# Kernel tuning notes

Measured on AMD Instinct MI355X. Metric: run time of the kernel, lower is better.

Reference implementation:

```python
import jax, jax.numpy as jnp
from jax import lax
import numpy as np

N = 65536
D = 512
NUM_STEPS = 10
TIME_INTERVAL = 1.0


def setup_inputs() -> dict:
    key = jax.random.key(0)
    ks = jax.random.split(key, 8)
    s1 = 1.0 / np.sqrt(D + 1)
    s2 = 1.0 / np.sqrt(D)
    sg = 1.0 / np.sqrt(2 * D)
    return {
        "current_node_features": jax.random.normal(ks[0], (N, D), jnp.float32),
        "previous_hidden_state": jax.random.normal(ks[1], (N, D), jnp.float32),
        # torch nn.Linear layout: weight [out, in], bias [out]
        "W1": jax.random.uniform(ks[2], (D, D + 1), jnp.float32, -s1, s1),
        "b1": jax.random.uniform(ks[3], (D,), jnp.float32, -s1, s1),
        "W2": jax.random.uniform(ks[4], (D, D), jnp.float32, -s2, s2),
        "b2": jax.random.uniform(ks[5], (D,), jnp.float32, -s2, s2),
        "Wg": jax.random.uniform(ks[6], (D, 2 * D), jnp.float32, -sg, sg),
        "bg": jax.random.uniform(ks[7], (D,), jnp.float32, -sg, sg),
    }


def reference(current_node_features, previous_hidden_state, W1, b1, W2, b2, Wg, bg):
    x = current_node_features
    dt = jnp.asarray(TIME_INTERVAL / NUM_STEPS, x.dtype)
    n = x.shape[0]

    def euler_step(h, t):
        # concat time feature: [N, D+1]
        time_col = jnp.full((n, 1), t, h.dtype)
        z = jnp.concatenate([h, time_col], axis=-1)
        deriv = jnp.tanh(jnp.tanh(z @ W1.T + b1) @ W2.T + b2)
        return h + dt * deriv, None

    ts = jnp.arange(NUM_STEPS, dtype=x.dtype) * dt  # t_i = start + i*dt
    evolved, _ = lax.scan(euler_step, previous_hidden_state, ts)

    combined = jnp.concatenate([x, evolved], axis=-1)  # [N, 2D]
    gate = jax.nn.sigmoid(combined @ Wg.T + bg)
    updated = gate * evolved + (1.0 - gate) * x
    return updated, updated
```

## Files before the change

kernel.cpp:

```cpp
#include <hip/hip_runtime.h>

#define N_ROWS 65536
#define DIM    512
#define NSTEP  10

typedef float  f32x16 __attribute__((ext_vector_type(16)));
typedef float  f32x4  __attribute__((ext_vector_type(4)));
typedef short  s16x8  __attribute__((ext_vector_type(8)));
typedef __bf16 bf16x8 __attribute__((ext_vector_type(8)));
typedef unsigned int u32x2 __attribute__((ext_vector_type(2)));
typedef unsigned int u32x4 __attribute__((ext_vector_type(4)));

__device__ __forceinline__ unsigned f2bf(float f) {
  unsigned u = __float_as_uint(f);
  return (u + 0x7fffu + ((u >> 16) & 1u)) >> 16;
}
__device__ __forceinline__ unsigned pack2bf_rn(float a, float b) {
  unsigned ua = __float_as_uint(a) + 0x8000u;
  unsigned ub = __float_as_uint(b) + 0x8000u;
  return __builtin_amdgcn_perm(ub, ua, 0x07060302u);
}
#define LOG2E_X2 2.885390081777927f
#define LOG2E    1.442695040888963f
__device__ __forceinline__ float ftanh(float x) {
  float t = __builtin_amdgcn_exp2f(x * LOG2E_X2);
  float r = __builtin_amdgcn_rcpf(1.0f + t);
  return __builtin_fmaf(-2.0f, r, 1.0f);
}
__device__ __forceinline__ float fsigm(float x) {
  float t = __builtin_amdgcn_exp2f(-x * LOG2E);
  return __builtin_amdgcn_rcpf(1.0f + t);
}
__device__ __forceinline__ void mfma(f32x16& c, s16x8 a, s16x8 b) {
  c = __builtin_amdgcn_mfma_f32_32x32x16_bf16(
        __builtin_bit_cast(bf16x8, a), __builtin_bit_cast(bf16x8, b), c, 0, 0, 0);
}

__global__ void pack_frags_kernel(const float* __restrict__ src, int row_stride,
                                  int col_off, unsigned short* __restrict__ dst) {
  const int idx = blockIdx.x * 256 + threadIdx.x;
  const int l    = idx & 63;
  const int frag = idx >> 6;
  const int otg  = frag >> 5;
  const int ks   = frag & 31;
  const int o = otg * 32 + (l & 31);
  const int k = ks * 16 + (l >> 5) * 8;
  const float* p = src + (size_t)o * row_stride + col_off + k;
  s16x8 v;
#pragma unroll
  for (int i = 0; i < 8; ++i) v[i] = (short)f2bf(p[i]);
  *reinterpret_cast<s16x8*>(dst + (size_t)idx * 8) = v;
}

__global__ void c1_kernel(const float* __restrict__ W1, const float* __restrict__ b1,
                          float* __restrict__ c1) {
  const int o = threadIdx.x;
  const float wt = W1[(size_t)o * 513 + 512];
  const float bb = b1[o];
  for (int s = 0; s < NSTEP; ++s)
    c1[s * DIM + o] = bb + ((float)s * 0.1f) * wt;
}

__global__ __launch_bounds__(512, 2)
void ode_fused(const float* __restrict__ x, const float* __restrict__ h0,
               const float* __restrict__ b2, const float* __restrict__ bg,
               const s16x8* __restrict__ w1f, const s16x8* __restrict__ w2f,
               const s16x8* __restrict__ wgaf, const s16x8* __restrict__ wgbf,
               const float* __restrict__ c1, float* __restrict__ out)
{
  __shared__ char ldsT[64 * 1024];

  const int tid = threadIdx.x;
  const int w   = tid >> 6;
  const int l   = tid & 63;
  const int lm  = l & 31;
  const int h5  = l >> 5;
  const int m0  = blockIdx.x << 6;
  const int ow  = w << 6;
  const unsigned lbyte = (unsigned)l << 4;

  {
#pragma unroll
    for (int q = 0; q < 8; ++q) {
      const int f  = (w << 3) | q;
      const int ks = f >> 1;
      const int mt = f & 1;
      const float* src = h0 + (size_t)(m0 + (mt << 5) + lm) * DIM + (ks << 4) + (h5 << 3);
      f32x4 v0 = *reinterpret_cast<const f32x4*>(src);
      f32x4 v1 = *reinterpret_cast<const f32x4*>(src + 4);
      u32x4 pk;
      pk[0] = pack2bf_rn(v0[0], v0[1]); pk[1] = pack2bf_rn(v0[2], v0[3]);
      pk[2] = pack2bf_rn(v1[0], v1[1]); pk[3] = pack2bf_rn(v1[2], v1[3]);
      *reinterpret_cast<u32x4*>(ldsT + (f << 10) + lbyte) = pk;
    }
  }

  f32x16 hst[2][2];
#pragma unroll
  for (int ot = 0; ot < 2; ++ot)
#pragma unroll
    for (int mt = 0; mt < 2; ++mt) {
      const float* hr = h0 + (size_t)(m0 + (mt << 5) + lm) * DIM;
#pragma unroll
      for (int g = 0; g < 4; ++g) {
        const int oc = ow + (ot << 5) + (g << 3) + (h5 << 2);
        f32x4 v = *reinterpret_cast<const f32x4*>(hr + oc);
#pragma unroll
        for (int j = 0; j < 4; ++j) hst[ot][mt][(g << 2) + j] = v[j];
      }
    }

  f32x16 acc[2][2];

  auto mm_lds = [&](const s16x8* __restrict__ A) {
    const s16x8* A0 = A + (w << 12);
    const s16x8* A1 = A0 + 2048;
    s16x8 a0[4], a1[4];
#pragma unroll
    for (int i = 0; i < 4; ++i) { a0[i] = A0[(i << 6) + l]; a1[i] = A1[(i << 6) + l]; }
#pragma unroll 4
    for (int ks = 0; ks < 28; ++ks) {
      s16x8 ca0 = a0[ks & 3], ca1 = a1[ks & 3];
      a0[ks & 3] = A0[((ks + 4) << 6) + l];
      a1[ks & 3] = A1[((ks + 4) << 6) + l];
      s16x8 b0 = *reinterpret_cast<const s16x8*>(ldsT + (ks << 11) + lbyte);
      s16x8 b1 = *reinterpret_cast<const s16x8*>(ldsT + (ks << 11) + 1024 + lbyte);
      mfma(acc[0][0], ca0, b0);
      mfma(acc[0][1], ca0, b1);
      mfma(acc[1][0], ca1, b0);
      mfma(acc[1][1], ca1, b1);
    }
#pragma unroll
    for (int ks = 28; ks < 32; ++ks) {
      s16x8 ca0 = a0[ks & 3], ca1 = a1[ks & 3];
      s16x8 b0 = *reinterpret_cast<const s16x8*>(ldsT + (ks << 11) + lbyte);
      s16x8 b1 = *reinterpret_cast<const s16x8*>(ldsT + (ks << 11) + 1024 + lbyte);
      mfma(acc[0][0], ca0, b0);
      mfma(acc[0][1], ca0, b1);
      mfma(acc[1][0], ca1, b0);
      mfma(acc[1][1], ca1, b1);
    }
  };

  auto acc_init = [&](const float* __restrict__ vec) {
#pragma unroll
    for (int ot = 0; ot < 2; ++ot)
#pragma unroll
      for (int g = 0; g < 4; ++g) {
        const int oc = ow + (ot << 5) + (g << 3) + (h5 << 2);
        f32x4 v = *reinterpret_cast<const f32x4*>(vec + oc);
#pragma unroll
        for (int mt = 0; mt < 2; ++mt)
#pragma unroll
          for (int j = 0; j < 4; ++j) acc[ot][mt][(g << 2) + j] = v[j];
      }
  };

  auto tile_write = [&](const f32x16 src[2][2]) {
    const unsigned base = ((unsigned)w << 13) + ((unsigned)lm << 4) + ((unsigned)h5 << 3);
#pragma unroll
    for (int ot = 0; ot < 2; ++ot)
#pragma unroll
      for (int mt = 0; mt < 2; ++mt)
#pragma unroll
        for (int g = 0; g < 4; ++g) {
          u32x2 pk;
          pk[0] = pack2bf_rn(src[ot][mt][(g << 2) + 0], src[ot][mt][(g << 2) + 1]);
          pk[1] = pack2bf_rn(src[ot][mt][(g << 2) + 2], src[ot][mt][(g << 2) + 3]);
          *reinterpret_cast<u32x2*>(ldsT + base + (ot << 12) + ((g >> 1) << 11)
                                    + (mt << 10) + ((g & 1) << 9)) = pk;
        }
  };

  __syncthreads();

#pragma unroll 1
  for (int s = 0; s < NSTEP; ++s) {
    acc_init(c1 + s * DIM);
    mm_lds(w1f);
#pragma unroll
    for (int ot = 0; ot < 2; ++ot)
#pragma unroll
      for (int mt = 0; mt < 2; ++mt)
#pragma unroll
        for (int i = 0; i < 16; ++i) acc[ot][mt][i] = ftanh(acc[ot][mt][i]);
    __syncthreads();
    tile_write(acc);
    __syncthreads();
    acc_init(b2);
    mm_lds(w2f);
#pragma unroll
    for (int ot = 0; ot < 2; ++ot)
#pragma unroll
      for (int mt = 0; mt < 2; ++mt)
#pragma unroll
        for (int i = 0; i < 16; ++i) {
          float t = __builtin_amdgcn_exp2f(acc[ot][mt][i] * LOG2E_X2);
          float r = __builtin_amdgcn_rcpf(1.0f + t);
          hst[ot][mt][i] = __builtin_fmaf(-0.2f, r, hst[ot][mt][i] + 0.1f);
        }
    __syncthreads();
    tile_write(hst);
    __syncthreads();
  }

  acc_init(bg);
  mm_lds(wgbf);
  {
    const s16x8* A0 = wgaf + (w << 12);
    const s16x8* A1 = A0 + 2048;
    const float* xr0 = x + (size_t)(m0 + lm) * DIM + (h5 << 3);
    const float* xr1 = xr0 + (size_t)32 * DIM;
#pragma unroll 4
    for (int ks = 0; ks < 32; ++ks) {
      s16x8 a0 = A0[(ks << 6) + l];
      s16x8 a1 = A1[(ks << 6) + l];
      const int kc = ks << 4;
      f32x4 u0 = *reinterpret_cast<const f32x4*>(xr0 + kc);
      f32x4 u1 = *reinterpret_cast<const f32x4*>(xr0 + kc + 4);
      u32x4 pb;
      pb[0] = pack2bf_rn(u0[0], u0[1]); pb[1] = pack2bf_rn(u0[2], u0[3]);
      pb[2] = pack2bf_rn(u1[0], u1[1]); pb[3] = pack2bf_rn(u1[2], u1[3]);
      s16x8 b0 = __builtin_bit_cast(s16x8, pb);
      f32x4 w0 = *reinterpret_cast<const f32x4*>(xr1 + kc);
      f32x4 w1 = *reinterpret_cast<const f32x4*>(xr1 + kc + 4);
      u32x4 qb;
      qb[0] = pack2bf_rn(w0[0], w0[1]); qb[1] = pack2bf_rn(w0[2], w0[3]);
      qb[2] = pack2bf_rn(w1[0], w1[1]); qb[3] = pack2bf_rn(w1[2], w1[3]);
      s16x8 b1 = __builtin_bit_cast(s16x8, qb);
      mfma(acc[0][0], a0, b0);
      mfma(acc[0][1], a0, b1);
      mfma(acc[1][0], a1, b0);
      mfma(acc[1][1], a1, b1);
    }
  }

  float* out1 = out + (size_t)N_ROWS * DIM;
#pragma unroll
  for (int mt = 0; mt < 2; ++mt) {
    const int m = m0 + (mt << 5) + lm;
    const float* xr = x + (size_t)m * DIM;
    float* o0p = out  + (size_t)m * DIM;
    float* o1p = out1 + (size_t)m * DIM;
#pragma unroll
    for (int ot = 0; ot < 2; ++ot)
#pragma unroll
      for (int g = 0; g < 4; ++g) {
        const int oc = ow + (ot << 5) + (g << 3) + (h5 << 2);
        f32x4 xv = *reinterpret_cast<const f32x4*>(xr + oc);
        f32x4 r;
#pragma unroll
        for (int j = 0; j < 4; ++j) {
          const float gt = fsigm(acc[ot][mt][(g << 2) + j]);
          const float ev = hst[ot][mt][(g << 2) + j];
          r[j] = gt * ev + (1.0f - gt) * xv[j];
        }
        *reinterpret_cast<f32x4*>(o0p + oc) = r;
        *reinterpret_cast<f32x4*>(o1p + oc) = r;
      }
  }
}

extern "C" void kernel_launch(void* const* d_in, const int* in_sizes, int n_in,
                              void* d_out, int out_size, void* d_ws, size_t ws_size,
                              hipStream_t stream) {
  const float* x  = (const float*)d_in[0];
  const float* h0 = (const float*)d_in[1];
  const float* W1 = (const float*)d_in[2];
  const float* b1 = (const float*)d_in[3];
  const float* W2 = (const float*)d_in[4];
  const float* b2 = (const float*)d_in[5];
  const float* Wg = (const float*)d_in[6];
  const float* bg = (const float*)d_in[7];

  char* ws = (char*)d_ws;
  const size_t FRAG_BYTES = (size_t)512 * 512 * 2;
  unsigned short* w1f  = (unsigned short*)(ws + 0 * FRAG_BYTES);
  unsigned short* w2f  = (unsigned short*)(ws + 1 * FRAG_BYTES);
  unsigned short* wgaf = (unsigned short*)(ws + 2 * FRAG_BYTES);
  unsigned short* wgbf = (unsigned short*)(ws + 3 * FRAG_BYTES);
  float*          c1   = (float*)(ws + 4 * FRAG_BYTES);

  pack_frags_kernel<<<128, 256, 0, stream>>>(W1, 513, 0,   w1f);
  pack_frags_kernel<<<128, 256, 0, stream>>>(W2, 512, 0,   w2f);
  pack_frags_kernel<<<128, 256, 0, stream>>>(Wg, 1024, 0,  wgaf);
  pack_frags_kernel<<<128, 256, 0, stream>>>(Wg, 1024, 512, wgbf);
  c1_kernel<<<1, 512, 0, stream>>>(W1, b1, c1);

  ode_fused<<<N_ROWS / 64, 512, 0, stream>>>(x, h0, b2, bg,
                                             (const s16x8*)w1f, (const s16x8*)w2f,
                                             (const s16x8*)wgaf, (const s16x8*)wgbf,
                                             c1, (float*)d_out);
}
```

Before: 1.054 ms.

## Double-buffer LDS activation tiles to drop per-step barriers

Splits the single 64KB LDS tile into two ping-pong buffers (ldsA/ldsB). Each GEMM now reads one buffer while its output goes to the other, which removes two of the four __syncthreads per Euler step. It also drops the manual 4-deep register prefetch of weight fragments in the GEMM loop and lowers the unroll of the gate loop from 4 to 2. The cost is 128KB of LDS per block, which likely no longer fits two blocks per CU as launch_bounds(512,2) asks, so occupancy and latency hiding may drop.

```diff
diff --git a/kernel.cpp b/kernel.cpp
--- a/kernel.cpp
+++ b/kernel.cpp
@@ -68,7 +68,8 @@
                const s16x8* __restrict__ wgaf, const s16x8* __restrict__ wgbf,
                const float* __restrict__ c1, float* __restrict__ out)
 {
-  __shared__ char ldsT[64 * 1024];
+  __shared__ char ldsA[64 * 1024];
+  __shared__ char ldsB[64 * 1024];
 
   const int tid = threadIdx.x;
   const int w   = tid >> 6;
@@ -91,7 +92,7 @@
       u32x4 pk;
       pk[0] = pack2bf_rn(v0[0], v0[1]); pk[1] = pack2bf_rn(v0[2], v0[3]);
       pk[2] = pack2bf_rn(v1[0], v1[1]); pk[3] = pack2bf_rn(v1[2], v1[3]);
-      *reinterpret_cast<u32x4*>(ldsT + (f << 10) + lbyte) = pk;
+      *reinterpret_cast<u32x4*>(ldsA + (f << 10) + lbyte) = pk;
     }
   }
 
@@ -112,33 +113,19 @@
 
   f32x16 acc[2][2];
 
-  auto mm_lds = [&](const s16x8* __restrict__ A) {
+  auto mm_lds = [&](const s16x8* __restrict__ A, const char* __restrict__ buf) {
     const s16x8* A0 = A + (w << 12);
     const s16x8* A1 = A0 + 2048;
-    s16x8 a0[4], a1[4];
-#pragma unroll
-    for (int i = 0; i < 4; ++i) { a0[i] = A0[(i << 6) + l]; a1[i] = A1[(i << 6) + l]; }
 #pragma unroll 4
-    for (int ks = 0; ks < 28; ++ks) {
-      s16x8 ca0 = a0[ks & 3], ca1 = a1[ks & 3];
-      a0[ks & 3] = A0[((ks + 4) << 6) + l];
-      a1[ks & 3] = A1[((ks + 4) << 6) + l];
-      s16x8 b0 = *reinterpret_cast<const s16x8*>(ldsT + (ks << 11) + lbyte);
-      s16x8 b1 = *reinterpret_cast<const s16x8*>(ldsT + (ks << 11) + 1024 + lbyte);
-      mfma(acc[0][0], ca0, b0);
-      mfma(acc[0][1], ca0, b1);
-      mfma(acc[1][0], ca1, b0);
-      mfma(acc[1][1], ca1, b1);
-    }
-#pragma unroll
-    for (int ks = 28; ks < 32; ++ks) {
-      s16x8 ca0 = a0[ks & 3], ca1 = a1[ks & 3];
-      s16x8 b0 = *reinterpret_cast<const s16x8*>(ldsT + (ks << 11) + lbyte);
-      s16x8 b1 = *reinterpret_cast<const s16x8*>(ldsT + (ks << 11) + 1024 + lbyte);
-      mfma(acc[0][0], ca0, b0);
-      mfma(acc[0][1], ca0, b1);
-      mfma(acc[1][0], ca1, b0);
-      mfma(acc[1][1], ca1, b1);
+    for (int ks = 0; ks < 32; ++ks) {
+      s16x8 a0 = A0[(ks << 6) + l];
+      s16x8 a1 = A1[(ks << 6) + l];
+      s16x8 b0 = *reinterpret_cast<const s16x8*>(buf + (ks << 11) + lbyte);
+      s16x8 b1 = *reinterpret_cast<const s16x8*>(buf + (ks << 11) + 1024 + lbyte);
+      mfma(acc[0][0], a0, b0);
+      mfma(acc[0][1], a0, b1);
+      mfma(acc[1][0], a1, b0);
+      mfma(acc[1][1], a1, b1);
     }
   };
 
@@ -156,7 +143,7 @@
       }
   };
 
-  auto tile_write = [&](const f32x16 src[2][2]) {
+  auto tile_write = [&](const f32x16 src[2][2], char* __restrict__ buf) {
     const unsigned base = ((unsigned)w << 13) + ((unsigned)lm << 4) + ((unsigned)h5 << 3);
 #pragma unroll
     for (int ot = 0; ot < 2; ++ot)
@@ -167,7 +154,7 @@
           u32x2 pk;
           pk[0] = pack2bf_rn(src[ot][mt][(g << 2) + 0], src[ot][mt][(g << 2) + 1]);
           pk[1] = pack2bf_rn(src[ot][mt][(g << 2) + 2], src[ot][mt][(g << 2) + 3]);
-          *reinterpret_cast<u32x2*>(ldsT + base + (ot << 12) + ((g >> 1) << 11)
+          *reinterpret_cast<u32x2*>(buf + base + (ot << 12) + ((g >> 1) << 11)
                                     + (mt << 10) + ((g & 1) << 9)) = pk;
         }
   };
@@ -177,18 +164,17 @@
 #pragma unroll 1
   for (int s = 0; s < NSTEP; ++s) {
     acc_init(c1 + s * DIM);
-    mm_lds(w1f);
+    mm_lds(w1f, ldsA);
 #pragma unroll
     for (int ot = 0; ot < 2; ++ot)
 #pragma unroll
       for (int mt = 0; mt < 2; ++mt)
 #pragma unroll
         for (int i = 0; i < 16; ++i) acc[ot][mt][i] = ftanh(acc[ot][mt][i]);
-    __syncthreads();
-    tile_write(acc);
+    tile_write(acc, ldsB);
     __syncthreads();
     acc_init(b2);
-    mm_lds(w2f);
+    mm_lds(w2f, ldsB);
 #pragma unroll
     for (int ot = 0; ot < 2; ++ot)
 #pragma unroll
@@ -199,19 +185,18 @@
           float r = __builtin_amdgcn_rcpf(1.0f + t);
           hst[ot][mt][i] = __builtin_fmaf(-0.2f, r, hst[ot][mt][i] + 0.1f);
         }
+    tile_write(hst, ldsA);
     __syncthreads();
-    tile_write(hst);
-    __syncthreads();
   }
 
   acc_init(bg);
-  mm_lds(wgbf);
+  mm_lds(wgbf, ldsA);
   {
     const s16x8* A0 = wgaf + (w << 12);
     const s16x8* A1 = A0 + 2048;
     const float* xr0 = x + (size_t)(m0 + lm) * DIM + (h5 << 3);
     const float* xr1 = xr0 + (size_t)32 * DIM;
-#pragma unroll 4
+#pragma unroll 2
     for (int ks = 0; ks < 32; ++ks) {
       s16x8 a0 = A0[(ks << 6) + l];
       s16x8 a1 = A1[(ks << 6) + l];
```

Measured after the change: 1.002 ms. -5.0%, faster.
